# Optimization experiments

Hardware: AMD Instinct MI355X
Metric: run time of the kernel (lower is better)

## Reference

```python
import jax, jax.numpy as jnp
import numpy as np

IN_F = 4096
OUT_F = 4096
RANK = 8
ALPHA = 8
SCALE = ALPHA / RANK


def setup_inputs() -> dict:
    key = jax.random.key(0)
    kx, kw, kb, ka = jax.random.split(key, 4)
    x = jax.random.normal(kx, (4, 4096, IN_F), dtype=jnp.float32)
    # base frozen linear params (torch Linear default init style, any values ok)
    W = jax.random.normal(kw, (OUT_F, IN_F), dtype=jnp.float32) * (1.0 / np.sqrt(IN_F))
    b = jax.random.normal(kb, (OUT_F,), dtype=jnp.float32) * 0.01
    # lora_A: kaiming_uniform_(a=sqrt(5)) -> U(-bound, bound), bound = sqrt(6/((1+5)*in_f)) = 1/sqrt(in_f)
    bound = 1.0 / np.sqrt(IN_F)
    lora_A = jax.random.uniform(ka, (RANK, IN_F), dtype=jnp.float32, minval=-bound, maxval=bound)
    # lora_B initialized to zeros per module; use small random values so the LoRA path is exercised
    lora_B = jax.random.normal(jax.random.fold_in(key, 7), (OUT_F, RANK), dtype=jnp.float32) * 0.02
    return {"x": x, "W": W, "b": b, "lora_A": lora_A, "lora_B": lora_B}


def reference(x, W, b, lora_A, lora_B):
    # base: x @ W.T + b  [B,S,out_f]
    base = jnp.einsum("bsi,oi->bso", x, W) + b
    # low-rank path: (x @ A.T) @ B.T * scale
    xa = jnp.einsum("bsi,ri->bsr", x, lora_A)  # [B,S,r]
    lora = jnp.einsum("bsr,or->bso", xa, lora_B)
    return base + lora * SCALE
```

## Files before the change

### kernel.cpp

```cpp
#include <hip/hip_runtime.h>
#include <cstdint>

#define K_IN   4096
#define N_OUT  4096
#define M_ROWS 16384
#define RANK   8
#define LSCALE 1.0f
#define NT     64
#define ROWB   8192
#define AHALF  1048576

typedef __attribute__((ext_vector_type(8))) short  short8;
typedef __attribute__((ext_vector_type(4))) float  floatx4;

__device__ __forceinline__ unsigned short f2bf(float f) {
  uint32_t u = __float_as_uint(f);
  u += 0x7FFFu + ((u >> 16) & 1u);
  return (unsigned short)(u >> 16);
}

__global__ __launch_bounds__(256) void fold_w_kernel(
    const float* __restrict__ W, const float* __restrict__ lA,
    const float* __restrict__ lB, unsigned short* __restrict__ Weff) {
  int idx = blockIdx.x * 256 + threadIdx.x;
  int o = idx >> 10;
  int k = (idx & 1023) << 2;
  float4 w = *reinterpret_cast<const float4*>(W + (size_t)o * K_IN + k);
#pragma unroll
  for (int r = 0; r < RANK; ++r) {
    float s = LSCALE * lB[o * RANK + r];
    float4 a = *reinterpret_cast<const float4*>(lA + r * K_IN + k);
    w.x += s * a.x; w.y += s * a.y; w.z += s * a.z; w.w += s * a.w;
  }
  ushort4 p;
  p.x = f2bf(w.x); p.y = f2bf(w.y); p.z = f2bf(w.z); p.w = f2bf(w.w);
  *reinterpret_cast<ushort4*>(Weff + (size_t)o * K_IN + k) = p;
}

__global__ __launch_bounds__(256) void cvt_x_kernel(
    const float* __restrict__ x, unsigned short* __restrict__ xb) {
  size_t i = ((size_t)blockIdx.x * 256 + threadIdx.x) * 8;
  float4 a = *reinterpret_cast<const float4*>(x + i);
  float4 c = *reinterpret_cast<const float4*>(x + i + 4);
  uint4 v;
  v.x = (uint32_t)f2bf(a.x) | ((uint32_t)f2bf(a.y) << 16);
  v.y = (uint32_t)f2bf(a.z) | ((uint32_t)f2bf(a.w) << 16);
  v.z = (uint32_t)f2bf(c.x) | ((uint32_t)f2bf(c.y) << 16);
  v.w = (uint32_t)f2bf(c.z) | ((uint32_t)f2bf(c.w) << 16);
  *reinterpret_cast<uint4*>(xb + i) = v;
}

__device__ __forceinline__ void gload_lds16(const void* g, void* l) {
  __builtin_amdgcn_global_load_lds(
      (const __attribute__((address_space(1))) void*)g,
      (__attribute__((address_space(3))) void*)l, 16, 0, 0);
}

__global__ __launch_bounds__(512, 2) void gemm_kernel(
    const unsigned short* __restrict__ Xb, const unsigned short* __restrict__ Wb,
    const float* __restrict__ bias, float* __restrict__ out) {
  __shared__ alignas(16) char lds[2 * 65536];

  const int tid  = threadIdx.x;
  const int wave = tid >> 6, lane = tid & 63;
  const int wr = wave >> 2, wc = wave & 3;
  const int l15 = lane & 15, sq = lane >> 4;

  int bx  = blockIdx.x;
  int sbx = (bx & 7) * 128 + (bx >> 3);
  const int mt = sbx >> 4;
  const int nt = sbx & 15;

  const int rstg = tid >> 3;
  const int cbst = ((tid & 7) << 4) ^ (tid & 32);
  const char* aBase = (const char*)Xb + (size_t)(mt * 256 + rstg) * ROWB + cbst;
  const char* bBase = (const char*)Wb + (size_t)(nt * 256 + rstg) * ROWB + cbst;

#define STAGE(H) do {                                                     \
    int th_ = (H) >> 2, hh_ = (H) & 3;                                    \
    const char* src_ = ((hh_ < 2) ? aBase + (size_t)hh_ * AHALF           \
                                  : bBase + (size_t)(hh_ - 2) * AHALF)    \
                       + th_ * 128;                                       \
    char* dst_ = lds + (th_ & 1) * 65536 + hh_ * 16384 + tid * 16;        \
    gload_lds16(src_, dst_);                                              \
    gload_lds16(src_ + (size_t)64 * ROWB, dst_ + 8192);                   \
  } while (0)
#define BAR() do { asm volatile("" ::: "memory");                         \
    __builtin_amdgcn_s_barrier();                                         \
    asm volatile("" ::: "memory"); } while (0)
#define LDSWZ(ROW, COLB) ((((ROW) << 7) | (COLB)) ^ (((ROW) & 4) << 3))
#define LOAD_A(DST, MQ) do {                                              \
    const char* Ab_ = lds + tb + wr * 16384;                              \
    _Pragma("unroll")                                                     \
    for (int ks = 0; ks < 2; ++ks)                                        \
      _Pragma("unroll")                                                   \
      for (int fi = 0; fi < 4; ++fi) {                                    \
        int row_ = (MQ) * 64 + fi * 16 + l15;                             \
        int cb_  = ks * 64 + sq * 16;                                     \
        DST[ks * 4 + fi] =                                                \
            *reinterpret_cast<const short8*>(Ab_ + LDSWZ(row_, cb_));     \
      } } while (0)
#define LOAD_B(DST, NQ) do {                                              \
    const char* Bb_ = lds + tb + (2 + (wc >> 1)) * 16384;                 \
    _Pragma("unroll")                                                     \
    for (int ks = 0; ks < 2; ++ks)                                        \
      _Pragma("unroll")                                                   \
      for (int fj = 0; fj < 2; ++fj) {                                    \
        int row_ = (wc & 1) * 64 + (NQ) * 32 + fj * 16 + l15;             \
        int cb_  = ks * 64 + sq * 16;                                     \
        DST[ks * 2 + fj] =                                                \
            *reinterpret_cast<const short8*>(Bb_ + LDSWZ(row_, cb_));     \
      } } while (0)
#define MFMA_Q(MQ, NQ, AF, BF) do {                                       \
    __builtin_amdgcn_s_setprio(1);                                        \
    _Pragma("unroll")                                                     \
    for (int ks = 0; ks < 2; ++ks)                                        \
      _Pragma("unroll")                                                   \
      for (int fi = 0; fi < 4; ++fi)                                      \
        _Pragma("unroll")                                                 \
        for (int fj = 0; fj < 2; ++fj)                                    \
          acc[(MQ) * 4 + fi][(NQ) * 2 + fj] =                             \
              __builtin_amdgcn_mfma_f32_16x16x32_bf16(                    \
                  AF[ks * 4 + fi], BF[ks * 2 + fj],                       \
                  acc[(MQ) * 4 + fi][(NQ) * 2 + fj], 0, 0, 0);            \
    __builtin_amdgcn_s_setprio(0); } while (0)

  floatx4 acc[8][4];
#pragma unroll
  for (int i = 0; i < 8; ++i)
#pragma unroll
    for (int j = 0; j < 4; ++j)
      acc[i][j] = (floatx4){0.f, 0.f, 0.f, 0.f};

  for (int h = 0; h < 7; ++h) STAGE(h);
  asm volatile("s_waitcnt vmcnt(6)" ::: "memory");
  BAR();

  short8 afA[8], afB[8], bfC[4];

  for (int t = 0; t < NT; ++t) {
    const int tb = (t & 1) * 65536;
    const int p0 = 4 * t;

    LOAD_A(afA, 0);
    LOAD_B(bfC, 0);
    if (p0 + 7 < 4 * NT) STAGE(p0 + 7);
    BAR();
    MFMA_Q(0, 0, afA, bfC);
    BAR();

    LOAD_A(afB, 1);
    if (p0 + 8 < 4 * NT) STAGE(p0 + 8);
    BAR();
    MFMA_Q(1, 0, afB, bfC);
    BAR();

    LOAD_B(bfC, 1);
    if (p0 + 9 < 4 * NT) STAGE(p0 + 9);
    BAR();
    MFMA_Q(1, 1, afB, bfC);
    BAR();

    if (p0 + 10 < 4 * NT) STAGE(p0 + 10);
    if (t <= NT - 3)      asm volatile("s_waitcnt vmcnt(6)" ::: "memory");
    else if (t == NT - 2) asm volatile("s_waitcnt vmcnt(0)" ::: "memory");
    BAR();
    MFMA_Q(0, 1, afA, bfC);
    BAR();
  }
#undef STAGE
#undef LOAD_A
#undef LOAD_B
#undef MFMA_Q

  const int row0 = mt * 256 + wr * 128 + sq * 4;
  const int col0 = nt * 256 + wc * 64 + l15;
#pragma unroll
  for (int j = 0; j < 4; ++j) {
    int col = col0 + j * 16;
    float bv = bias[col];
#pragma unroll
    for (int i = 0; i < 8; ++i) {
      int rowb = row0 + i * 16;
#pragma unroll
      for (int rr = 0; rr < 4; ++rr)
        out[(size_t)(rowb + rr) * N_OUT + col] = acc[i][j][rr] + bv;
    }
  }
}

__global__ __launch_bounds__(256) void fallback_kernel(
    const float* __restrict__ x, const float* __restrict__ W,
    const float* __restrict__ bias, const float* __restrict__ lA,
    const float* __restrict__ lB, float* __restrict__ out) {
  __shared__ float Xs[64][17];
  __shared__ float Ws[64][17];
  int tid = threadIdx.x;
  int tx = tid & 15, ty = tid >> 4;
  int bm = blockIdx.y * 64, bn = blockIdx.x * 64;
  float acc[4][4] = {};
  for (int k0 = 0; k0 < K_IN; k0 += 16) {
#pragma unroll
    for (int q = 0; q < 4; ++q) {
      int flat = q * 256 + tid;
      int r = flat >> 4, c = flat & 15;
      Xs[r][c] = x[(size_t)(bm + r) * K_IN + k0 + c];
      float w = W[(size_t)(bn + r) * K_IN + k0 + c];
#pragma unroll
      for (int rr = 0; rr < RANK; ++rr)
        w += LSCALE * lB[(bn + r) * RANK + rr] * lA[rr * K_IN + k0 + c];
      Ws[r][c] = w;
    }
    __syncthreads();
#pragma unroll
    for (int kk = 0; kk < 16; ++kk) {
      float av[4], bv[4];
#pragma unroll
      for (int i = 0; i < 4; ++i) av[i] = Xs[ty * 4 + i][kk];
#pragma unroll
      for (int j = 0; j < 4; ++j) bv[j] = Ws[tx * 4 + j][kk];
#pragma unroll
      for (int i = 0; i < 4; ++i)
#pragma unroll
        for (int j = 0; j < 4; ++j) acc[i][j] += av[i] * bv[j];
    }
    __syncthreads();
  }
#pragma unroll
  for (int i = 0; i < 4; ++i)
#pragma unroll
    for (int j = 0; j < 4; ++j)
      out[(size_t)(bm + ty * 4 + i) * N_OUT + bn + tx * 4 + j] =
          acc[i][j] + bias[bn + tx * 4 + j];
}

extern "C" void kernel_launch(void* const* d_in, const int* in_sizes, int n_in,
                              void* d_out, int out_size, void* d_ws, size_t ws_size,
                              hipStream_t stream) {
  const float* x  = (const float*)d_in[0];
  const float* W  = (const float*)d_in[1];
  const float* b  = (const float*)d_in[2];
  const float* lA = (const float*)d_in[3];
  const float* lB = (const float*)d_in[4];
  float* out = (float*)d_out;

  const size_t weff_bytes = (size_t)N_OUT * K_IN * 2;
  const size_t xb_bytes   = (size_t)M_ROWS * K_IN * 2;

  if (ws_size >= weff_bytes + xb_bytes) {
    unsigned short* Weff = (unsigned short*)d_ws;
    unsigned short* Xb   = (unsigned short*)((char*)d_ws + weff_bytes);
    fold_w_kernel<<<(int)(((size_t)N_OUT * K_IN / 4) / 256), 256, 0, stream>>>(W, lA, lB, Weff);
    cvt_x_kernel<<<(int)(((size_t)M_ROWS * K_IN / 8) / 256), 256, 0, stream>>>(x, Xb);
    gemm_kernel<<<(M_ROWS / 256) * (N_OUT / 256), 512, 0, stream>>>(Xb, Weff, b, out);
  } else {
    dim3 grid(N_OUT / 64, M_ROWS / 64);
    fallback_kernel<<<grid, 256, 0, stream>>>(x, W, b, lA, lB, out);
  }
}
```

Measured before the change: 630.3 us.

## Split GEMM into 256-tile and 128-tile kernels and use full XOR LDS swizzle

The single 256x256-tile GEMM launch of 1024 blocks is replaced by two launches. The first covers rows 0-8191 with 256x256 tiles in 512 blocks. The second covers rows 8192-16383 with 128x128 tiles in 2048 blocks of 256 threads. The LDS swizzle changes from a single-bit XOR to a full 3-bit row XOR, aiming to remove bank conflicts on the fragment reads. The split appears meant to reduce wave-quantization tail effects across the CUs, but the smaller tiles reuse each loaded element less and add a second kernel launch.

After: 683.1 us. 1.08x slower.

```diff
diff --git a/kernel.cpp b/kernel.cpp
--- a/kernel.cpp
+++ b/kernel.cpp
@@ -56,7 +56,13 @@
       (__attribute__((address_space(3))) void*)l, 16, 0, 0);
 }
 
-__global__ __launch_bounds__(512, 2) void gemm_kernel(
+#define LDSWZ2(ROW, CB) (((ROW) << 7) | ((CB) ^ (((ROW) & 7) << 4)))
+#define BAR() do { asm volatile("" ::: "memory");                         \
+    __builtin_amdgcn_s_barrier();                                         \
+    asm volatile("" ::: "memory"); } while (0)
+#define LGKM0() asm volatile("s_waitcnt lgkmcnt(0)" ::: "memory")
+
+__global__ __launch_bounds__(512, 2) void gemm256_kernel(
     const unsigned short* __restrict__ Xb, const unsigned short* __restrict__ Wb,
     const float* __restrict__ bias, float* __restrict__ out) {
   __shared__ alignas(16) char lds[2 * 65536];
@@ -67,12 +73,12 @@
   const int l15 = lane & 15, sq = lane >> 4;
 
   int bx  = blockIdx.x;
-  int sbx = (bx & 7) * 128 + (bx >> 3);
+  int sbx = (bx & 7) * 64 + (bx >> 3);
   const int mt = sbx >> 4;
   const int nt = sbx & 15;
 
   const int rstg = tid >> 3;
-  const int cbst = ((tid & 7) << 4) ^ (tid & 32);
+  const int cbst = (((tid & 7) ^ ((tid >> 3) & 7)) << 4);
   const char* aBase = (const char*)Xb + (size_t)(mt * 256 + rstg) * ROWB + cbst;
   const char* bBase = (const char*)Wb + (size_t)(nt * 256 + rstg) * ROWB + cbst;
 
@@ -85,10 +91,6 @@
     gload_lds16(src_, dst_);                                              \
     gload_lds16(src_ + (size_t)64 * ROWB, dst_ + 8192);                   \
   } while (0)
-#define BAR() do { asm volatile("" ::: "memory");                         \
-    __builtin_amdgcn_s_barrier();                                         \
-    asm volatile("" ::: "memory"); } while (0)
-#define LDSWZ(ROW, COLB) ((((ROW) << 7) | (COLB)) ^ (((ROW) & 4) << 3))
 #define LOAD_A(DST, MQ) do {                                              \
     const char* Ab_ = lds + tb + wr * 16384;                              \
     _Pragma("unroll")                                                     \
@@ -98,7 +100,7 @@
         int row_ = (MQ) * 64 + fi * 16 + l15;                             \
         int cb_  = ks * 64 + sq * 16;                                     \
         DST[ks * 4 + fi] =                                                \
-            *reinterpret_cast<const short8*>(Ab_ + LDSWZ(row_, cb_));     \
+            *reinterpret_cast<const short8*>(Ab_ + LDSWZ2(row_, cb_));    \
       } } while (0)
 #define LOAD_B(DST, NQ) do {                                              \
     const char* Bb_ = lds + tb + (2 + (wc >> 1)) * 16384;                 \
@@ -109,7 +111,7 @@
         int row_ = (wc & 1) * 64 + (NQ) * 32 + fj * 16 + l15;             \
         int cb_  = ks * 64 + sq * 16;                                     \
         DST[ks * 2 + fj] =                                                \
-            *reinterpret_cast<const short8*>(Bb_ + LDSWZ(row_, cb_));     \
+            *reinterpret_cast<const short8*>(Bb_ + LDSWZ2(row_, cb_));    \
       } } while (0)
 #define MFMA_Q(MQ, NQ, AF, BF) do {                                       \
     __builtin_amdgcn_s_setprio(1);                                        \
@@ -189,6 +191,108 @@
   }
 }
 
+__global__ __launch_bounds__(256) void gemm128_kernel(
+    const unsigned short* __restrict__ Xb, const unsigned short* __restrict__ Wb,
+    const float* __restrict__ bias, float* __restrict__ out) {
+  __shared__ alignas(16) char lds[2 * 32768];
+
+  const int tid  = threadIdx.x;
+  const int wave = tid >> 6, lane = tid & 63;
+  const int wr = wave >> 1, wc = wave & 1;
+  const int l15 = lane & 15, sq = lane >> 4;
+
+  int bx  = blockIdx.x;
+  int sbx = (bx & 7) * 256 + (bx >> 3);
+  const int mt = sbx >> 5;
+  const int nt = sbx & 31;
+
+  const int rstg = tid >> 3;
+  const int cbst = (((tid & 7) ^ ((tid >> 3) & 7)) << 4);
+  const char* aBase = (const char*)Xb +
+      (size_t)(8192 + mt * 128 + rstg) * ROWB + cbst;
+  const char* bBase = (const char*)Wb + (size_t)(nt * 128 + rstg) * ROWB + cbst;
+
+#define STAGE2(TT) do {                                                   \
+    char* d_ = lds + ((TT) & 1) * 32768 + tid * 16;                       \
+    _Pragma("unroll")                                                     \
+    for (int q = 0; q < 4; ++q) {                                         \
+      gload_lds16(aBase + (TT) * 128 + (size_t)(q * 32) * ROWB,           \
+                  d_ + q * 4096);                                         \
+      gload_lds16(bBase + (TT) * 128 + (size_t)(q * 32) * ROWB,           \
+                  d_ + 16384 + q * 4096);                                 \
+    } } while (0)
+
+  floatx4 acc[4][4];
+#pragma unroll
+  for (int i = 0; i < 4; ++i)
+#pragma unroll
+    for (int j = 0; j < 4; ++j)
+      acc[i][j] = (floatx4){0.f, 0.f, 0.f, 0.f};
+
+  STAGE2(0); STAGE2(1);
+  asm volatile("s_waitcnt vmcnt(8)" ::: "memory");
+  BAR();
+
+  for (int t = 0; t < NT; ++t) {
+    const int tb = (t & 1) * 32768;
+
+    short8 af[8], bf[8];
+    {
+      const char* Ab_ = lds + tb;
+      const char* Bb_ = lds + tb + 16384;
+#pragma unroll
+      for (int ks = 0; ks < 2; ++ks)
+#pragma unroll
+        for (int f = 0; f < 4; ++f) {
+          int rowA = wr * 64 + f * 16 + l15;
+          int rowB = wc * 64 + f * 16 + l15;
+          int cb   = ks * 64 + sq * 16;
+          af[ks * 4 + f] =
+              *reinterpret_cast<const short8*>(Ab_ + LDSWZ2(rowA, cb));
+          bf[ks * 4 + f] =
+              *reinterpret_cast<const short8*>(Bb_ + LDSWZ2(rowB, cb));
+        }
+    }
+    LGKM0();
+    __builtin_amdgcn_s_setprio(1);
+#pragma unroll
+    for (int ks = 0; ks < 2; ++ks)
+#pragma unroll
+      for (int fi = 0; fi < 4; ++fi)
+#pragma unroll
+        for (int fj = 0; fj < 4; ++fj)
+          acc[fi][fj] = __builtin_amdgcn_mfma_f32_16x16x32_bf16(
+              af[ks * 4 + fi], bf[ks * 4 + fj], acc[fi][fj], 0, 0, 0);
+    __builtin_amdgcn_s_setprio(0);
+    BAR();
+
+    if (t + 2 < NT) {
+      STAGE2(t + 2);
+      asm volatile("s_waitcnt vmcnt(8)" ::: "memory");
+      BAR();
+    } else if (t + 1 < NT) {
+      asm volatile("s_waitcnt vmcnt(0)" ::: "memory");
+      BAR();
+    }
+  }
+#undef STAGE2
+
+  const int row0 = 8192 + mt * 128 + wr * 64 + sq * 4;
+  const int col0 = nt * 128 + wc * 64 + l15;
+#pragma unroll
+  for (int fj = 0; fj < 4; ++fj) {
+    int col = col0 + fj * 16;
+    float bv = bias[col];
+#pragma unroll
+    for (int fi = 0; fi < 4; ++fi) {
+      int rowb = row0 + fi * 16;
+#pragma unroll
+      for (int rr = 0; rr < 4; ++rr)
+        out[(size_t)(rowb + rr) * N_OUT + col] = acc[fi][fj][rr] + bv;
+    }
+  }
+}
+
 __global__ __launch_bounds__(256) void fallback_kernel(
     const float* __restrict__ x, const float* __restrict__ W,
     const float* __restrict__ bias, const float* __restrict__ lA,
@@ -252,7 +356,8 @@
     unsigned short* Xb   = (unsigned short*)((char*)d_ws + weff_bytes);
     fold_w_kernel<<<(int)(((size_t)N_OUT * K_IN / 4) / 256), 256, 0, stream>>>(W, lA, lB, Weff);
     cvt_x_kernel<<<(int)(((size_t)M_ROWS * K_IN / 8) / 256), 256, 0, stream>>>(x, Xb);
-    gemm_kernel<<<(M_ROWS / 256) * (N_OUT / 256), 512, 0, stream>>>(Xb, Weff, b, out);
+    gemm256_kernel<<<512, 512, 0, stream>>>(Xb, Weff, b, out);
+    gemm128_kernel<<<2048, 256, 0, stream>>>(Xb, Weff, b, out);
   } else {
     dim3 grid(N_OUT / 64, M_ROWS / 64);
     fallback_kernel<<<grid, 256, 0, stream>>>(x, W, b, lA, lB, out);
```
